# Optimization experiments

Measured on AMD Instinct MI355X. Metric: run time of the kernel, lower is better.

## Reference

```python
import jax, jax.numpy as jnp
import numpy as np

NW = 4096      # num_words in document
H = 768        # encoder hidden size
NC = 49152     # number of candidate spans
MSW = 30       # max_span_width
E = 20         # span width embedding size
M = 1024       # mlp hidden size
SPAN_EMB = 3 * H + E  # ment_emb='attn' -> start + end + attn term + width emb
NEG = -1e10


def setup_inputs() -> dict:
    key = jax.random.key(0)
    ks = jax.random.split(key, 16)
    s = 0.02
    encoded_doc = jax.random.normal(ks[0], (NW, H), jnp.float32)
    cand_starts = jax.random.randint(ks[1], (NC,), 0, NW - MSW)
    widths = jax.random.randint(ks[2], (NC,), 0, MSW)
    cand_ends = cand_starts + widths  # guaranteed < NW
    return {
        "encoded_doc": encoded_doc,
        "cand_starts": cand_starts,
        "cand_ends": cand_ends,
        "width_emb": jax.random.normal(ks[3], (MSW, E), jnp.float32) * s,
        "width_prior_emb": jax.random.normal(ks[4], (MSW, E), jnp.float32) * s,
        "attn_w": jax.random.normal(ks[5], (H,), jnp.float32) * s,
        "attn_b": jnp.zeros((1,), jnp.float32),
        "mlp1_w": jax.random.normal(ks[6], (SPAN_EMB, M), jnp.float32) * s,
        "mlp1_b": jnp.zeros((M,), jnp.float32),
        "mlp2_w": jax.random.normal(ks[7], (M,), jnp.float32) * s,
        "mlp2_b": jnp.zeros((1,), jnp.float32),
        "wmlp1_w": jax.random.normal(ks[8], (E, M), jnp.float32) * s,
        "wmlp1_b": jnp.zeros((M,), jnp.float32),
        "wmlp2_w": jax.random.normal(ks[9], (M,), jnp.float32) * s,
        "wmlp2_b": jnp.zeros((1,), jnp.float32),
    }


def reference(encoded_doc, cand_starts, cand_ends, width_emb, width_prior_emb,
              attn_w, attn_b, mlp1_w, mlp1_b, mlp2_w, mlp2_b,
              wmlp1_w, wmlp1_b, wmlp2_w, wmlp2_b):
    # span width index (clamped), shared by both width embedding tables
    width_idx = jnp.clip(cand_ends - cand_starts, 0, MSW - 1)

    # --- get_span_embeddings ---
    start_emb = encoded_doc[cand_starts]                 # [NC, H]
    end_emb = encoded_doc[cand_ends]                     # [NC, H]
    w_emb = width_emb[width_idx]                         # [NC, E]

    word_attn = encoded_doc @ attn_w + attn_b[0]         # [NW]
    doc_range = jnp.arange(NW)
    ment_mask = (doc_range[None, :] >= cand_starts[:, None]) & \
                (doc_range[None, :] <= cand_ends[:, None])       # [NC, NW]
    # original: (1 - mask)*-1e10 + word_attn
    scores = jnp.where(ment_mask, 0.0, NEG) + word_attn[None, :]
    mention_word_attn = jax.nn.softmax(scores, axis=1)   # [NC, NW]
    attention_term = mention_word_attn @ encoded_doc     # [NC, H]

    span_emb = jnp.concatenate([start_emb, end_emb, w_emb, attention_term],
                               axis=1)                   # [NC, 3H+E]

    # --- mention_mlp scoring (1 hidden ReLU layer -> scalar) ---
    h = jax.nn.relu(span_emb @ mlp1_w + mlp1_b)          # [NC, M]
    mention_logits = h @ mlp2_w + mlp2_b[0]              # [NC]

    # --- get_mention_width_scores ---
    wp = width_prior_emb[width_idx]                      # [NC, E]
    hw = jax.nn.relu(wp @ wmlp1_w + wmlp1_b)             # [NC, M]
    width_scores = hw @ wmlp2_w + wmlp2_b[0]             # [NC]

    return mention_logits + width_scores
```

## Files before the change

kernel.cpp:

```cpp
#include <hip/hip_runtime.h>
#include <math.h>

#define NW 4096
#define H 768
#define NC 49152
#define MSW 30
#define E 20
#define M 1024
#define CHUNK 64
#define NCH (NW / CHUNK)
#define NKT (H / 64)

typedef short bf16x8 __attribute__((ext_vector_type(8)));
typedef unsigned short u16x8 __attribute__((ext_vector_type(8)));
typedef float f32x4 __attribute__((ext_vector_type(4)));

__device__ __forceinline__ unsigned short f2bf(float x) {
    unsigned u = __float_as_uint(x);
    return (unsigned short)((u + 0x7fff + ((u >> 16) & 1)) >> 16);
}
__device__ __forceinline__ float bf2f(unsigned short b) {
    return __uint_as_float(((unsigned)b) << 16);
}
__device__ __forceinline__ void gload16(const void* g, void* l) {
    __builtin_amdgcn_global_load_lds((const __attribute__((address_space(1))) void*)g,
                                     (__attribute__((address_space(3))) void*)l, 16, 0, 0);
}

__global__ __launch_bounds__(256) void k_prep(const float* __restrict__ doc,
                                              const float* __restrict__ attn_w,
                                              const float* __restrict__ attn_b,
                                              unsigned short* __restrict__ docb,
                                              float* __restrict__ ewa,
                                              int* __restrict__ hist,
                                              const float* __restrict__ mlp1_w,
                                              unsigned short* __restrict__ Bt,
                                              const float* __restrict__ width_emb,
                                              const float* __restrict__ mlp1_b,
                                              float* __restrict__ PW,
                                              const float* __restrict__ wp_emb,
                                              const float* __restrict__ w1,
                                              const float* __restrict__ b1,
                                              const float* __restrict__ w2,
                                              const float* __restrict__ b2,
                                              float* __restrict__ wscore) {
    __shared__ float sh[32][33];
    __shared__ float red[256];
    int bx = blockIdx.x;
    int tid = threadIdx.x;
    if (bx < 1024) {
        if (bx < 16) hist[bx * 256 + tid] = 0;
        int row = bx * 4 + (tid >> 6);
        int lane = tid & 63;
        const float* r = doc + (size_t)row * H;
        float s = 0.f;
        #pragma unroll
        for (int q = 0; q < 3; ++q) {
            int idx = q * 256 + lane * 4;
            float4 v = *reinterpret_cast<const float4*>(r + idx);
            float4 w = *reinterpret_cast<const float4*>(attn_w + idx);
            s += v.x * w.x + v.y * w.y + v.z * w.z + v.w * w.w;
            ushort4 o;
            o.x = f2bf(v.x); o.y = f2bf(v.y); o.z = f2bf(v.z); o.w = f2bf(v.w);
            *reinterpret_cast<ushort4*>(docb + (size_t)row * H + idx) = o;
        }
        #pragma unroll
        for (int off = 32; off > 0; off >>= 1) s += __shfl_down(s, off);
        if (lane == 0) ewa[row] = expf(s + attn_b[0]);
    } else if (bx < 3328) {
        int idx = bx - 1024;
        int k0 = (idx % 24) * 32;
        int m0 = ((idx / 24) % 32) * 32;
        int part = idx / (24 * 32);
        int rb = part == 0 ? 0 : (part == 1 ? H : (2 * H + E));
        int tx = tid & 31, ty = tid >> 5;
        #pragma unroll
        for (int it = 0; it < 4; ++it) {
            int kk = ty + it * 8;
            sh[kk][tx] = mlp1_w[(size_t)(rb + k0 + kk) * M + m0 + tx];
        }
        __syncthreads();
        #pragma unroll
        for (int it = 0; it < 4; ++it) {
            int mm = ty + it * 8;
            Bt[(size_t)(part * M + m0 + mm) * H + k0 + tx] = f2bf(sh[tx][mm]);
        }
    } else {
        int idx = bx - 3328;
        int w = idx / 5, y = idx % 5;
        if (y < 4) {
            int m = y * 256 + tid;
            float acc = mlp1_b[m];
            #pragma unroll
            for (int e = 0; e < E; ++e)
                acc += width_emb[w * E + e] * mlp1_w[(size_t)(2 * H + e) * M + m];
            PW[w * M + m] = acc;
        } else {
            float part = 0.f;
            for (int m = tid; m < M; m += 256) {
                float h = b1[m];
                #pragma unroll
                for (int e = 0; e < E; ++e) h += wp_emb[w * E + e] * w1[e * M + m];
                part += fmaxf(h, 0.f) * w2[m];
            }
            red[tid] = part;
            __syncthreads();
            for (int s = 128; s > 0; s >>= 1) {
                if (tid < s) red[tid] += red[tid + s];
                __syncthreads();
            }
            if (tid == 0) wscore[w] = red[0] + b2[0];
        }
    }
}

__global__ __launch_bounds__(256) void k_scans2(const float* __restrict__ ewa,
                                                float* __restrict__ Dpre,
                                                const int* __restrict__ hist,
                                                int* __restrict__ offs,
                                                int* __restrict__ begs) {
    __shared__ float shf[256];
    __shared__ int shi[256];
    int t = threadIdx.x;
    if (blockIdx.x == 0) {
        float v[16];
        float sum = 0.f;
        #pragma unroll
        for (int i = 0; i < 16; ++i) { v[i] = ewa[t * 16 + i]; sum += v[i]; }
        shf[t] = sum;
        __syncthreads();
        for (int off = 1; off < 256; off <<= 1) {
            float x = (t >= off) ? shf[t - off] : 0.f;
            __syncthreads();
            shf[t] += x;
            __syncthreads();
        }
        float run = shf[t] - sum;
        #pragma unroll
        for (int i = 0; i < 16; ++i) { run += v[i]; Dpre[t * 16 + i + 1] = run; }
        if (t == 0) Dpre[0] = 0.f;
    } else {
        int v[16];
        int sum = 0;
        #pragma unroll
        for (int i = 0; i < 16; ++i) { v[i] = hist[t * 16 + i]; sum += v[i]; }
        shi[t] = sum;
        __syncthreads();
        for (int off = 1; off < 256; off <<= 1) {
            int x = (t >= off) ? shi[t - off] : 0;
            __syncthreads();
            shi[t] += x;
            __syncthreads();
        }
        int run = shi[t] - sum;
        #pragma unroll
        for (int i = 0; i < 16; ++i) {
            offs[t * 16 + i] = run;
            begs[t * 16 + i] = run;
            run += v[i];
        }
        if (t == 255) begs[4096] = run;
    }
}

__global__ __launch_bounds__(256) void k_hist(const int* __restrict__ starts,
                                              int* __restrict__ hist) {
    atomicAdd(&hist[starts[blockIdx.x * 256 + threadIdx.x]], 1);
}
__global__ __launch_bounds__(256) void k_scatter(const int* __restrict__ starts,
                                                 int* __restrict__ offs,
                                                 int* __restrict__ perm) {
    int c = blockIdx.x * 256 + threadIdx.x;
    int p = atomicAdd(&offs[starts[c]], 1);
    perm[p] = c;
}

__global__ __launch_bounds__(512, 2) void k_proj_mfma(const unsigned short* __restrict__ docb,
                                                      const unsigned short* __restrict__ Bt,
                                                      const float* __restrict__ ewa,
                                                      unsigned short* __restrict__ Pse,
                                                      float* __restrict__ Sbuf,
                                                      float* __restrict__ T) {
    __shared__ unsigned short As[2][16384];
    __shared__ unsigned short Bs[2][12288];
    int tid = threadIdx.x;
    int bid = blockIdx.x;
    int xcd = bid & 7, rr0 = bid >> 3;
    int coltile = (xcd & 1) * 8 + (rr0 & 7);
    int rowtile = (xcd >> 1) * 4 + (rr0 >> 3);
    int col0 = coltile * 192;
    int row0 = rowtile * 256;
    int wv = tid >> 6, lane = tid & 63;
    int wr = wv >> 2, wc = wv & 3;

    f32x4 acc[8][3];
    #pragma unroll
    for (int mi = 0; mi < 8; ++mi)
        #pragma unroll
        for (int ni = 0; ni < 3; ++ni) acc[mi][ni] = (f32x4){0.f, 0.f, 0.f, 0.f};

    #define STAGE(buf, k0)                                                            \
        {                                                                             \
            _Pragma("unroll")                                                         \
            for (int i = 0; i < 4; ++i) {                                             \
                int s = i * 512 + tid;                                                \
                int mg = s >> 7, ks = (s >> 6) & 1, g = (s >> 4) & 3, ri = s & 15;    \
                gload16(docb + (size_t)(row0 + mg * 16 + ri) * H + (k0) + ks * 32 + g * 8, \
                        (char*)As[buf] + s * 16);                                     \
            }                                                                         \
            _Pragma("unroll")                                                         \
            for (int i = 0; i < 3; ++i) {                                             \
                int s = i * 512 + tid;                                                \
                int cg = s >> 7, ks = (s >> 6) & 1, g = (s >> 4) & 3, ci = s & 15;    \
                gload16(Bt + (size_t)(col0 + cg * 16 + ci) * H + (k0) + ks * 32 + g * 8, \
                        (char*)Bs[buf] + s * 16);                                     \
            }                                                                         \
        }

    STAGE(0, 0);
    STAGE(1, 64);
    asm volatile("s_waitcnt vmcnt(7)" ::: "memory");
    __builtin_amdgcn_s_barrier();

    #pragma unroll 1
    for (int t = 0; t < NKT; ++t) {
        int cur = t & 1;
        bf16x8 af[2][8], bfr[2][3];
        #pragma unroll
        for (int ks = 0; ks < 2; ++ks) {
            #pragma unroll
            for (int mi = 0; mi < 8; ++mi)
                af[ks][mi] = *reinterpret_cast<const bf16x8*>(
                    (char*)As[cur] + (wr * 8 + mi) * 2048 + ks * 1024 + lane * 16);
            #pragma unroll
            for (int ni = 0; ni < 3; ++ni)
                bfr[ks][ni] = *reinterpret_cast<const bf16x8*>(
                    (char*)Bs[cur] + (wc * 3 + ni) * 2048 + ks * 1024 + lane * 16);
        }
        __builtin_amdgcn_s_setprio(1);
        #pragma unroll
        for (int ks = 0; ks < 2; ++ks)
            #pragma unroll
            for (int mi = 0; mi < 8; ++mi)
                #pragma unroll
                for (int ni = 0; ni < 3; ++ni)
                    acc[mi][ni] = __builtin_amdgcn_mfma_f32_16x16x32_bf16(
                        af[ks][mi], bfr[ks][ni], acc[mi][ni], 0, 0, 0);
        __builtin_amdgcn_s_setprio(0);
        if (t + 2 < NKT) {
            asm volatile("s_waitcnt lgkmcnt(0)" ::: "memory");
            __builtin_amdgcn_sched_barrier(0);
            __builtin_amdgcn_s_barrier();
            STAGE(cur, (t + 2) * 64);
            asm volatile("s_waitcnt vmcnt(7)" ::: "memory");
            __builtin_amdgcn_s_barrier();
        } else if (t + 2 == NKT) {
            asm volatile("s_waitcnt vmcnt(0)" ::: "memory");
            __builtin_amdgcn_s_barrier();
        }
    }
    #undef STAGE

    int cr = (lane >> 4) * 4;
    int cc = lane & 15;
    #pragma unroll
    for (int mi = 0; mi < 8; ++mi) {
        #pragma unroll
        for (int ni = 0; ni < 3; ++ni) {
            int rrow = row0 + wr * 128 + mi * 16 + cr;
            int cabs = col0 + wc * 48 + ni * 16 + cc;
            int part = cabs >> 10;
            int cm = cabs & 1023;
            if (part < 2) {
                unsigned short* dst = Pse + (size_t)rrow * 2048 + part * 1024 + cm;
                #pragma unroll
                for (int j = 0; j < 4; ++j) dst[(size_t)j * 2048] = f2bf(acc[mi][ni][j]);
            } else {
                float* dst = Sbuf + (size_t)rrow * M + cm;
                #pragma unroll
                for (int j = 0; j < 4; ++j) dst[(size_t)j * M] = acc[mi][ni][j];
            }
        }
    }
    #pragma unroll
    for (int half = 0; half < 2; ++half) {
        int chunk = (row0 >> 6) + wr * 2 + half;
        #pragma unroll
        for (int ni = 0; ni < 3; ++ni) {
            int cabs = col0 + wc * 48 + ni * 16 + cc;
            if (cabs >= 2048) {
                float psum = 0.f;
                #pragma unroll
                for (int mi4 = 0; mi4 < 4; ++mi4) {
                    int mi = half * 4 + mi4;
                    int rbase = row0 + wr * 128 + mi * 16 + cr;
                    #pragma unroll
                    for (int j = 0; j < 4; ++j)
                        psum += ewa[rbase + j] * acc[mi][ni][j];
                }
                psum += __shfl_down(psum, 16);
                psum += __shfl_down(psum, 32);
                if ((lane >> 4) == 0)
                    T[(size_t)chunk * M + (cabs - 2048)] = psum;
            }
        }
    }
}

__global__ __launch_bounds__(256) void k_scan2(float* __restrict__ T) {
    int m = blockIdx.x * 256 + threadIdx.x;
    float v[NCH];
    #pragma unroll
    for (int c = 0; c < NCH; ++c) v[c] = T[c * M + m];
    float run = 0.f;
    #pragma unroll
    for (int c = 0; c < NCH; ++c) { float t = v[c]; T[c * M + m] = run; run += t; }
}

__global__ __launch_bounds__(256) void k_scan3(float* __restrict__ Sbuf,
                                               const float* __restrict__ ewa,
                                               const float* __restrict__ T) {
    int m = blockIdx.x * 256 + threadIdx.x;
    int c = blockIdx.y;
    __shared__ float ew[CHUNK];
    if (threadIdx.x < CHUNK) ew[threadIdx.x] = ewa[c * CHUNK + threadIdx.x];
    __syncthreads();
    float acc = T[c * M + m];
    float* base = Sbuf + (size_t)(c * CHUNK) * M + m;
    #pragma unroll 4
    for (int i = 0; i < CHUNK; ++i) {
        float* p = base + (size_t)i * M;
        acc += ew[i] * (*p);
        *p = acc;
    }
}

__global__ __launch_bounds__(256) void k_cand(const unsigned short* __restrict__ Pse,
                                              const float* __restrict__ Sbuf,
                                              const float* __restrict__ PW,
                                              const float* __restrict__ Dpre,
                                              const float* __restrict__ wscore,
                                              const int* __restrict__ perm,
                                              const int* __restrict__ begs,
                                              const int* __restrict__ ends,
                                              const float* __restrict__ mlp2_w,
                                              const float* __restrict__ mlp2_b,
                                              float* __restrict__ out) {
    __shared__ __align__(16) unsigned short ps_l[1024];
    __shared__ __align__(16) float ss_l[1024];
    int bid = blockIdx.x;
    int s = (bid & 7) * 512 + (bid >> 3);
    int tid = threadIdx.x;
    {
        ushort4 p4 = *reinterpret_cast<const ushort4*>(Pse + (size_t)s * 2048 + tid * 4);
        *reinterpret_cast<ushort4*>(ps_l + tid * 4) = p4;
        float4 s4 = (s > 0) ? *reinterpret_cast<const float4*>(Sbuf + (size_t)(s - 1) * M + tid * 4)
                            : make_float4(0.f, 0.f, 0.f, 0.f);
        *reinterpret_cast<float4*>(ss_l + tid * 4) = s4;
    }
    __syncthreads();
    int beg = begs[s], end = begs[s + 1];
    int wv = tid >> 6, lane = tid & 63;
    float dps = Dpre[s];
    float4 v00 = *reinterpret_cast<const float4*>(mlp2_w + lane * 8);
    float4 v01 = *reinterpret_cast<const float4*>(mlp2_w + lane * 8 + 4);
    float4 v10 = *reinterpret_cast<const float4*>(mlp2_w + lane * 8 + 512);
    float4 v11 = *reinterpret_cast<const float4*>(mlp2_w + lane * 8 + 516);

    for (int j = beg + wv; j < end; j += 4) {
        int c = perm[j];
        int e = ends[c];
        int wi = e - s;
        wi = wi > MSW - 1 ? MSW - 1 : wi;
        float inv = 1.f / (Dpre[e + 1] - dps);
        const unsigned short* pe = Pse + (size_t)e * 2048 + 1024;
        const float* se = Sbuf + (size_t)e * M;
        const float* pw = PW + (size_t)wi * M;

        float part = 0.f;
        #pragma unroll
        for (int q = 0; q < 2; ++q) {
            int m = lane * 8 + q * 512;
            u16x8 a8 = *reinterpret_cast<const u16x8*>(ps_l + m);
            u16x8 b8 = *reinterpret_cast<const u16x8*>(pe + m);
            float4 t0 = *reinterpret_cast<const float4*>(se + m);
            float4 t1 = *reinterpret_cast<const float4*>(se + m + 4);
            float4 u0 = *reinterpret_cast<const float4*>(ss_l + m);
            float4 u1 = *reinterpret_cast<const float4*>(ss_l + m + 4);
            float4 w0 = *reinterpret_cast<const float4*>(pw + m);
            float4 w1 = *reinterpret_cast<const float4*>(pw + m + 4);
            float4 v0 = q ? v10 : v00;
            float4 v1 = q ? v11 : v01;
            float x;
            x = bf2f(a8[0]) + bf2f(b8[0]) + w0.x + (t0.x - u0.x) * inv; part += fmaxf(x, 0.f) * v0.x;
            x = bf2f(a8[1]) + bf2f(b8[1]) + w0.y + (t0.y - u0.y) * inv; part += fmaxf(x, 0.f) * v0.y;
            x = bf2f(a8[2]) + bf2f(b8[2]) + w0.z + (t0.z - u0.z) * inv; part += fmaxf(x, 0.f) * v0.z;
            x = bf2f(a8[3]) + bf2f(b8[3]) + w0.w + (t0.w - u0.w) * inv; part += fmaxf(x, 0.f) * v0.w;
            x = bf2f(a8[4]) + bf2f(b8[4]) + w1.x + (t1.x - u1.x) * inv; part += fmaxf(x, 0.f) * v1.x;
            x = bf2f(a8[5]) + bf2f(b8[5]) + w1.y + (t1.y - u1.y) * inv; part += fmaxf(x, 0.f) * v1.y;
            x = bf2f(a8[6]) + bf2f(b8[6]) + w1.z + (t1.z - u1.z) * inv; part += fmaxf(x, 0.f) * v1.z;
            x = bf2f(a8[7]) + bf2f(b8[7]) + w1.w + (t1.w - u1.w) * inv; part += fmaxf(x, 0.f) * v1.w;
        }
        #pragma unroll
        for (int off = 32; off > 0; off >>= 1) part += __shfl_down(part, off);
        if (lane == 0) out[c] = part + mlp2_b[0] + wscore[wi];
    }
}

extern "C" void kernel_launch(void* const* d_in, const int* in_sizes, int n_in,
                              void* d_out, int out_size, void* d_ws, size_t ws_size,
                              hipStream_t stream) {
    const float* encoded_doc = (const float*)d_in[0];
    const int*   cand_starts = (const int*)d_in[1];
    const int*   cand_ends   = (const int*)d_in[2];
    const float* width_emb   = (const float*)d_in[3];
    const float* width_prior = (const float*)d_in[4];
    const float* attn_w      = (const float*)d_in[5];
    const float* attn_b      = (const float*)d_in[6];
    const float* mlp1_w      = (const float*)d_in[7];
    const float* mlp1_b      = (const float*)d_in[8];
    const float* mlp2_w      = (const float*)d_in[9];
    const float* mlp2_b      = (const float*)d_in[10];
    const float* wmlp1_w     = (const float*)d_in[11];
    const float* wmlp1_b     = (const float*)d_in[12];
    const float* wmlp2_w     = (const float*)d_in[13];
    const float* wmlp2_b     = (const float*)d_in[14];
    float* out = (float*)d_out;

    float* Sbuf   = (float*)d_ws;
    float* T      = Sbuf + (size_t)NW * M;
    float* PW     = T + NCH * M;
    float* ewa    = PW + MSW * M;
    float* Dpre   = ewa + NW;
    float* wscore = Dpre + 4160;
    unsigned short* Pse  = (unsigned short*)(wscore + 64);
    unsigned short* docb = Pse + (size_t)NW * 2048;
    unsigned short* Btb  = docb + (size_t)NW * H;
    int* hist = (int*)(Btb + (size_t)3072 * H);
    int* offs = hist + 4096;
    int* begs = offs + 4096;
    int* perm = begs + 4112;

    k_prep<<<3478, 256, 0, stream>>>(encoded_doc, attn_w, attn_b, docb, ewa, hist,
                                     mlp1_w, Btb, width_emb, mlp1_b, PW,
                                     width_prior, wmlp1_w, wmlp1_b, wmlp2_w, wmlp2_b, wscore);
    k_hist<<<NC / 256, 256, 0, stream>>>(cand_starts, hist);
    k_scans2<<<2, 256, 0, stream>>>(ewa, Dpre, hist, offs, begs);
    k_scatter<<<NC / 256, 256, 0, stream>>>(cand_starts, offs, perm);
    k_proj_mfma<<<256, 512, 0, stream>>>(docb, Btb, ewa, Pse, Sbuf, T);
    k_scan2<<<M / 256, 256, 0, stream>>>(T);
    k_scan3<<<dim3(M / 256, NCH), 256, 0, stream>>>(Sbuf, ewa, T);
    k_cand<<<4096, 256, 0, stream>>>(Pse, Sbuf, PW, Dpre, wscore, perm, begs,
                                     cand_ends, mlp2_w, mlp2_b, out);
}
```

Before: 110.6 us.

## Switch projection GEMM to 32x32x16 MFMA with 4x2 wave tiling

Replaces the 16x16x32 bf16 MFMA tiles with 32x32x16 tiles in the projection GEMM. The wave layout changes from 2x4 to 4x2, the LDS staging layout is reorganised to match the new fragment shape, and the epilogue and chunk-sum reduction are remapped to the 16-register accumulator layout. Launch bounds drop to one block per CU. The aim is higher MFMA throughput per instruction and fewer LDS fragment reads, at the cost of occupancy and scattered per-row epilogue stores.

```diff
diff --git a/kernel.cpp b/kernel.cpp
--- a/kernel.cpp
+++ b/kernel.cpp
@@ -13,7 +13,7 @@
 
 typedef short bf16x8 __attribute__((ext_vector_type(8)));
 typedef unsigned short u16x8 __attribute__((ext_vector_type(8)));
-typedef float f32x4 __attribute__((ext_vector_type(4)));
+typedef float f32x16 __attribute__((ext_vector_type(16)));
 
 __device__ __forceinline__ unsigned short f2bf(float x) {
     unsigned u = __float_as_uint(x);
@@ -175,7 +175,7 @@
     perm[p] = c;
 }
 
-__global__ __launch_bounds__(512, 2) void k_proj_mfma(const unsigned short* __restrict__ docb,
+__global__ __launch_bounds__(512, 1) void k_proj_mfma(const unsigned short* __restrict__ docb,
                                                       const unsigned short* __restrict__ Bt,
                                                       const float* __restrict__ ewa,
                                                       unsigned short* __restrict__ Pse,
@@ -191,28 +191,32 @@
     int col0 = coltile * 192;
     int row0 = rowtile * 256;
     int wv = tid >> 6, lane = tid & 63;
-    int wr = wv >> 2, wc = wv & 3;
-
-    f32x4 acc[8][3];
+    int wr = wv >> 1, wc = wv & 1;
+
+    f32x16 acc[2][3];
     #pragma unroll
-    for (int mi = 0; mi < 8; ++mi)
-        #pragma unroll
-        for (int ni = 0; ni < 3; ++ni) acc[mi][ni] = (f32x4){0.f, 0.f, 0.f, 0.f};
+    for (int mi = 0; mi < 2; ++mi)
+        #pragma unroll
+        for (int ni = 0; ni < 3; ++ni)
+            #pragma unroll
+            for (int j = 0; j < 16; ++j) acc[mi][ni][j] = 0.f;
 
     #define STAGE(buf, k0)                                                            \
         {                                                                             \
             _Pragma("unroll")                                                         \
             for (int i = 0; i < 4; ++i) {                                             \
                 int s = i * 512 + tid;                                                \
-                int mg = s >> 7, ks = (s >> 6) & 1, g = (s >> 4) & 3, ri = s & 15;    \
-                gload16(docb + (size_t)(row0 + mg * 16 + ri) * H + (k0) + ks * 32 + g * 8, \
+                int mg = s >> 8, ks = (s >> 6) & 3, l = s & 63;                       \
+                gload16(docb + (size_t)(row0 + mg * 32 + (l & 31)) * H                \
+                              + (k0) + ks * 16 + (l >> 5) * 8,                        \
                         (char*)As[buf] + s * 16);                                     \
             }                                                                         \
             _Pragma("unroll")                                                         \
             for (int i = 0; i < 3; ++i) {                                             \
                 int s = i * 512 + tid;                                                \
-                int cg = s >> 7, ks = (s >> 6) & 1, g = (s >> 4) & 3, ci = s & 15;    \
-                gload16(Bt + (size_t)(col0 + cg * 16 + ci) * H + (k0) + ks * 32 + g * 8, \
+                int cg = s >> 8, ks = (s >> 6) & 3, l = s & 63;                       \
+                gload16(Bt + (size_t)(col0 + cg * 32 + (l & 31)) * H                  \
+                            + (k0) + ks * 16 + (l >> 5) * 8,                          \
                         (char*)Bs[buf] + s * 16);                                     \
             }                                                                         \
         }
@@ -225,28 +229,26 @@
     #pragma unroll 1
     for (int t = 0; t < NKT; ++t) {
         int cur = t & 1;
-        bf16x8 af[2][8], bfr[2][3];
-        #pragma unroll
-        for (int ks = 0; ks < 2; ++ks) {
+        #pragma unroll
+        for (int ks = 0; ks < 4; ++ks) {
+            bf16x8 af[2], bfr[3];
             #pragma unroll
-            for (int mi = 0; mi < 8; ++mi)
-                af[ks][mi] = *reinterpret_cast<const bf16x8*>(
-                    (char*)As[cur] + (wr * 8 + mi) * 2048 + ks * 1024 + lane * 16);
+            for (int mi = 0; mi < 2; ++mi)
+                af[mi] = *reinterpret_cast<const bf16x8*>(
+                    (char*)As[cur] + (((wr * 2 + mi) * 4 + ks) * 64 + lane) * 16);
             #pragma unroll
             for (int ni = 0; ni < 3; ++ni)
-                bfr[ks][ni] = *reinterpret_cast<const bf16x8*>(
-                    (char*)Bs[cur] + (wc * 3 + ni) * 2048 + ks * 1024 + lane * 16);
-        }
-        __builtin_amdgcn_s_setprio(1);
-        #pragma unroll
-        for (int ks = 0; ks < 2; ++ks)
+                bfr[ni] = *reinterpret_cast<const bf16x8*>(
+                    (char*)Bs[cur] + (((wc * 3 + ni) * 4 + ks) * 64 + lane) * 16);
+            __builtin_amdgcn_s_setprio(1);
             #pragma unroll
-            for (int mi = 0; mi < 8; ++mi)
+            for (int mi = 0; mi < 2; ++mi)
                 #pragma unroll
                 for (int ni = 0; ni < 3; ++ni)
-                    acc[mi][ni] = __builtin_amdgcn_mfma_f32_16x16x32_bf16(
-                        af[ks][mi], bfr[ks][ni], acc[mi][ni], 0, 0, 0);
-        __builtin_amdgcn_s_setprio(0);
+                    acc[mi][ni] = __builtin_amdgcn_mfma_f32_32x32x16_bf16(
+                        af[mi], bfr[ni], acc[mi][ni], 0, 0, 0);
+            __builtin_amdgcn_s_setprio(0);
+        }
         if (t + 2 < NKT) {
             asm volatile("s_waitcnt lgkmcnt(0)" ::: "memory");
             __builtin_amdgcn_sched_barrier(0);
@@ -261,46 +263,49 @@
     }
     #undef STAGE
 
-    int cr = (lane >> 4) * 4;
-    int cc = lane & 15;
+    int lcol = lane & 31;
+    int lrh = lane >> 5;
     #pragma unroll
-    for (int mi = 0; mi < 8; ++mi) {
+    for (int mi = 0; mi < 2; ++mi) {
         #pragma unroll
         for (int ni = 0; ni < 3; ++ni) {
-            int rrow = row0 + wr * 128 + mi * 16 + cr;
-            int cabs = col0 + wc * 48 + ni * 16 + cc;
+            int cabs = col0 + wc * 96 + ni * 32 + lcol;
             int part = cabs >> 10;
             int cm = cabs & 1023;
+            int rbase = row0 + wr * 64 + mi * 32 + 4 * lrh;
             if (part < 2) {
-                unsigned short* dst = Pse + (size_t)rrow * 2048 + part * 1024 + cm;
                 #pragma unroll
-                for (int j = 0; j < 4; ++j) dst[(size_t)j * 2048] = f2bf(acc[mi][ni][j]);
+                for (int reg = 0; reg < 16; ++reg) {
+                    int r = rbase + (reg & 3) + 8 * (reg >> 2);
+                    Pse[(size_t)r * 2048 + part * 1024 + cm] = f2bf(acc[mi][ni][reg]);
+                }
             } else {
-                float* dst = Sbuf + (size_t)rrow * M + cm;
                 #pragma unroll
-                for (int j = 0; j < 4; ++j) dst[(size_t)j * M] = acc[mi][ni][j];
+                for (int reg = 0; reg < 16; ++reg) {
+                    int r = rbase + (reg & 3) + 8 * (reg >> 2);
+                    Sbuf[(size_t)r * M + cm] = acc[mi][ni][reg];
+                }
             }
         }
     }
-    #pragma unroll
-    for (int half = 0; half < 2; ++half) {
-        int chunk = (row0 >> 6) + wr * 2 + half;
+    {
+        int chunk = (row0 >> 6) + wr;
         #pragma unroll
         for (int ni = 0; ni < 3; ++ni) {
-            int cabs = col0 + wc * 48 + ni * 16 + cc;
+            int cabs = col0 + wc * 96 + ni * 32 + lcol;
             if (cabs >= 2048) {
                 float psum = 0.f;
                 #pragma unroll
-                for (int mi4 = 0; mi4 < 4; ++mi4) {
-                    int mi = half * 4 + mi4;
-                    int rbase = row0 + wr * 128 + mi * 16 + cr;
+                for (int mi = 0; mi < 2; ++mi) {
+                    int rbase = row0 + wr * 64 + mi * 32 + 4 * lrh;
                     #pragma unroll
-                    for (int j = 0; j < 4; ++j)
-                        psum += ewa[rbase + j] * acc[mi][ni][j];
+                    for (int reg = 0; reg < 16; ++reg) {
+                        int r = rbase + (reg & 3) + 8 * (reg >> 2);
+                        psum += ewa[r] * acc[mi][ni][reg];
+                    }
                 }
-                psum += __shfl_down(psum, 16);
                 psum += __shfl_down(psum, 32);
-                if ((lane >> 4) == 0)
+                if (lrh == 0)
                     T[(size_t)chunk * M + (cabs - 2048)] = psum;
             }
         }
```

After: 111.3 us. No clear change (+0.7%).
